# Optimization experiments

Hardware: AMD Instinct MI355X
Metric: run time of the kernel (lower is better)

## Reference

```python
import jax, jax.numpy as jnp
from jax import lax
import numpy as np

RANK = 128
INPUT_DIM = 128
OUT_DIM = 32
N = 128
L = 512
INIT_STD = 1.0 / np.sqrt(RANK * INPUT_DIM)  # variance-preserving recurrence


def setup_inputs() -> dict:
    key = jax.random.key(0)
    k_x, k_A, k_a, k_O = jax.random.split(key, 4)
    x = jax.random.normal(k_x, (N, L, INPUT_DIM), dtype=jnp.float32)
    A = INIT_STD * jax.random.normal(k_A, (RANK, INPUT_DIM, RANK), dtype=jnp.float32)
    alpha = INIT_STD * jax.random.normal(k_a, (RANK,), dtype=jnp.float32)
    Omega = INIT_STD * jax.random.normal(k_O, (RANK, OUT_DIM), dtype=jnp.float32)
    return {"x": x, "alpha": alpha, "A": A, "Omega": Omega}


def reference(x, alpha, A, Omega):
    # x: [N, L, D]; alpha: [R]; A: [R, D, R]; Omega: [R, M]
    # h_0 = einsum('i,ijk,nj->nk', alpha, A, x[:,0])
    h0 = jnp.einsum('i,ijk,nj->nk', alpha, A, x[:, 0, :])

    def step(h, xt):
        # h: [N, R], xt: [N, D] -> new h: [N, R]
        h = jnp.einsum('ni,ijk,nj->nk', h, A, xt)
        return h, None

    xs = jnp.swapaxes(x, 0, 1)[1:]  # [L-1, N, D]
    h, _ = lax.scan(step, h0, xs)
    out = jnp.einsum('ni,im->nm', h, Omega)  # [N, M]
    return jnp.squeeze(out)
```

## Files before the change

### kernel.cpp

```cpp
#include <hip/hip_runtime.h>

typedef _Float16 f16;
typedef _Float16 half8 __attribute__((ext_vector_type(8)));
typedef _Float16 half4v __attribute__((ext_vector_type(4)));
typedef float f32x4 __attribute__((ext_vector_type(4)));


#define GLOAD_LDS16(g, l) __builtin_amdgcn_global_load_lds( \
    (const __attribute__((address_space(1))) void*)(g),     \
    (__attribute__((address_space(3))) void*)(l), 16, 0, 0)

__global__ void k_cvt_pre(const float* __restrict__ x, f16* __restrict__ Xh,
                          const float* __restrict__ A, f16* __restrict__ Af2) {
    int b = blockIdx.x;
    if (b < 256) {
        int tid = (b << 8) + threadIdx.x;
        int n = tid >> 9;
        int rem = tid & 511;
        int off = (n << 16) + (rem << 2);
        float4 v = *(const float4*)(x + off);
        half4v o; o[0] = (f16)v.x; o[1] = (f16)v.y; o[2] = (f16)v.z; o[3] = (f16)v.w;
        *(half4v*)(Xh + off) = o;
    } else {
        int o = ((b - 256) << 8) + threadIdx.x;
        int i = o >> 14, k = (o >> 7) & 127, j = o & 127;
        Af2[o] = (f16)A[(i << 14) + (j << 7) + k];
    }
}

__device__ __forceinline__
void gemm_body(f16* lA, f16* lX, const f16* __restrict__ Af2, const f16* __restrict__ Xh,
               f16* __restrict__ B, int t0, int logTc, int qtile, int i, int tid) {
    const int Tcm1 = (1 << logTc) - 1;
    const int rowidx = tid >> 4;
    const int cc = tid & 15;
    const int scc = cc ^ rowidx;
    const int wv = tid >> 6;

    {
        const f16* srcA = Af2 + ((size_t)i << 14);
#pragma unroll
        for (int r = 0; r < 128; r += 16) {
            GLOAD_LDS16(srcA + ((r + rowidx) << 7) + (scc << 3),
                        lA + ((r + (wv << 2)) << 7));
        }
#pragma unroll
        for (int r = 0; r < 128; r += 16) {
            int qr = (qtile << 7) + r + rowidx;
            int n = qr >> logTc;
            int trel = qr & Tcm1;
            GLOAD_LDS16(Xh + (((size_t)(n << 9) + t0 + trel) << 7) + (scc << 3),
                        lX + ((r + (wv << 2)) << 7));
        }
    }
    __syncthreads();

    const int lane = tid & 63;
    const int l15 = lane & 15;
    const int l4 = lane >> 4;
    f32x4 acc[8][2] = {};

#pragma unroll
    for (int ks = 0; ks < 4; ++ks) {
        const int c = (ks << 2) + l4;
        half8 afr[8], bfr[2];
#pragma unroll
        for (int mt = 0; mt < 8; ++mt) {
            int rowA = (mt << 4) + l15;
            afr[mt] = *(const half8*)(&lA[(rowA << 7) + ((c ^ l15) << 3)]);
        }
#pragma unroll
        for (int qt = 0; qt < 2; ++qt) {
            int rowX = (wv << 5) + (qt << 4) + l15;
            bfr[qt] = *(const half8*)(&lX[(rowX << 7) + ((c ^ l15) << 3)]);
        }
#pragma unroll
        for (int mt = 0; mt < 8; ++mt)
#pragma unroll
            for (int qt = 0; qt < 2; ++qt)
                acc[mt][qt] = __builtin_amdgcn_mfma_f32_16x16x32_f16(
                    afr[mt], bfr[qt], acc[mt][qt], 0, 0, 0);
    }

    __syncthreads();
    f16* stage = lA;
#pragma unroll
    for (int mt = 0; mt < 8; ++mt)
#pragma unroll
        for (int qt = 0; qt < 2; ++qt) {
            int q = (wv << 5) + (qt << 4) + l15;
            int chunk = (mt << 1) + (l4 >> 1);
            int hf = l4 & 1;
            half4v o;
            o[0] = (f16)acc[mt][qt][0];
            o[1] = (f16)acc[mt][qt][1];
            o[2] = (f16)acc[mt][qt][2];
            o[3] = (f16)acc[mt][qt][3];
            *(half4v*)(&stage[(q << 7) + (((chunk ^ l15) << 3) + (hf << 2))]) = o;
        }
    __syncthreads();
    {
        const int lr = lane >> 4;
        const int lc = lane & 15;
#pragma unroll
        for (int it = 0; it < 8; ++it) {
            int q = (wv << 5) + (it << 2) + lr;
            uint4 v = *(const uint4*)(&stage[(q << 7) + ((lc ^ (q & 15)) << 3)]);
            size_t qg = (size_t)((qtile << 7) + q);
            *(uint4*)(B + (qg << 14) + (i << 7) + (lc << 3)) = v;
        }
    }
}

__device__ __forceinline__
void chain_body(float* hl, float (*part)[132], const f16* __restrict__ B,
                float* __restrict__ hstate, const float* __restrict__ alpha,
                const float* __restrict__ Om, float* __restrict__ out,
                int Tc, int first, int last, int n, int tid) {
    const int kg = tid & 15;
    const int iq = tid >> 4;

    if (tid < 128) hl[tid] = first ? alpha[tid] : hstate[(n << 7) + tid];
    __syncthreads();

    const f16* bbase = B + (((size_t)n * Tc) << 14) + (iq << 10) + (kg << 3);
    half8 buf[4][8];
#pragma unroll
    for (int s = 0; s < 4; ++s)
#pragma unroll
        for (int ii = 0; ii < 8; ++ii)
            buf[s][ii] = *(const half8*)(bbase + ((size_t)s << 14) + (ii << 7));

    for (int t = 0; t < Tc; t += 4) {
#pragma unroll
        for (int s = 0; s < 4; ++s) {
            float4 h0 = *(const float4*)&hl[iq << 3];
            float4 h1 = *(const float4*)&hl[(iq << 3) + 4];
            float acc[8] = {0, 0, 0, 0, 0, 0, 0, 0};
#pragma unroll
            for (int ii = 0; ii < 4; ++ii) {
                float hv = (&h0.x)[ii];
#pragma unroll
                for (int j = 0; j < 8; ++j)
                    acc[j] += hv * (float)buf[s][ii][j];
            }
#pragma unroll
            for (int ii = 0; ii < 4; ++ii) {
                float hv = (&h1.x)[ii];
#pragma unroll
                for (int j = 0; j < 8; ++j)
                    acc[j] += hv * (float)buf[s][ii + 4][j];
            }
            int tn = t + s + 4;
            if (tn < Tc) {
#pragma unroll
                for (int ii = 0; ii < 8; ++ii)
                    buf[s][ii] = *(const half8*)(bbase + ((size_t)tn << 14) + (ii << 7));
            }
            *(float4*)(&part[iq][kg << 3])       = make_float4(acc[0], acc[1], acc[2], acc[3]);
            *(float4*)(&part[iq][(kg << 3) + 4]) = make_float4(acc[4], acc[5], acc[6], acc[7]);
            __syncthreads();
            if (tid < 128) {
                float s0 = part[0][tid] + part[1][tid];
                float s1 = part[2][tid] + part[3][tid];
                float s2 = part[4][tid] + part[5][tid];
                float s3 = part[6][tid] + part[7][tid];
                s0 += part[8][tid] + part[9][tid];
                s1 += part[10][tid] + part[11][tid];
                s2 += part[12][tid] + part[13][tid];
                s3 += part[14][tid] + part[15][tid];
                hl[tid] = (s0 + s1) + (s2 + s3);
            }
            __syncthreads();
        }
    }

    if (!last) {
        if (tid < 128) hstate[(n << 7) + tid] = hl[tid];
    } else if (tid < 32) {
        float s = 0.f;
        for (int i2 = 0; i2 < 128; ++i2) s += hl[i2] * Om[(i2 << 5) + tid];
        out[(n << 5) + tid] = s;
    }
}

__device__ __forceinline__ int chain_n(int bx, int logTc) {
    if (logTc == 4) return (bx & 64) | ((bx & 7) << 3) | ((bx >> 3) & 7);
    return bx;
}

__global__ __launch_bounds__(256, 2)
void k_gemm0(const f16* __restrict__ Af2, const f16* __restrict__ Xh,
             f16* __restrict__ B, const float* __restrict__ x, int logTc) {
    __shared__ __align__(16) char smem[65536];
    const int bx = blockIdx.x;
    const int Tc = 1 << logTc;
    const int ngemm = Tc << 7;
    if (bx < ngemm) {
        gemm_body((f16*)smem, (f16*)(smem + 32768), Af2, Xh, B, 0, logTc,
                  bx & (Tc - 1), bx >> logTc, threadIdx.x);
    } else {
        int f = ((bx - ngemm) << 8) + threadIdx.x;
        int t = (f & 16383) >> 5;
        if (t < 16) return;
        float4 v = *(const float4*)(x + ((size_t)f << 2));
        half4v o; o[0] = (f16)v.x; o[1] = (f16)v.y; o[2] = (f16)v.z; o[3] = (f16)v.w;
        *(half4v*)(Xh + ((size_t)f << 2)) = o;
    }
}

__global__ __launch_bounds__(256, 2)
void k_chain(const f16* __restrict__ B, float* __restrict__ hstate,
             const float* __restrict__ alpha, const float* __restrict__ Om,
             float* __restrict__ out, int Tc, int logTc, int first, int last) {
    __shared__ __align__(16) char smem[16384];
    chain_body((float*)smem, (float(*)[132])(smem + 512), B, hstate, alpha, Om, out,
               Tc, first, last, chain_n(blockIdx.x, logTc), threadIdx.x);
}

__global__ __launch_bounds__(256, 2)
void k_fused(const f16* __restrict__ Af2, const f16* __restrict__ Xh,
             f16* __restrict__ Bw, const f16* __restrict__ Br,
             float* __restrict__ hstate, const float* __restrict__ alpha,
             const float* __restrict__ Om, float* __restrict__ out,
             int t0g, int logTc, int Tc, int first, int last) {
    __shared__ __align__(16) char smem[65536];
    const int bx = blockIdx.x;
    if (bx < 128) {
        chain_body((float*)smem, (float(*)[132])(smem + 512), Br, hstate, alpha, Om, out,
                   Tc, first, last, chain_n(bx, logTc), threadIdx.x);
    } else {
        int g = bx - 128;
        int qtile = g & (Tc - 1);
        int i = g >> logTc;
        gemm_body((f16*)smem, (f16*)(smem + 32768), Af2, Xh, Bw, t0g, logTc,
                  qtile, i, threadIdx.x);
    }
}

extern "C" void kernel_launch(void* const* d_in, const int* in_sizes, int n_in,
                              void* d_out, int out_size, void* d_ws, size_t ws_size,
                              hipStream_t stream) {
    const float* x     = (const float*)d_in[0];
    const float* alpha = (const float*)d_in[1];
    const float* A     = (const float*)d_in[2];
    const float* Om    = (const float*)d_in[3];
    float* out = (float*)d_out;

    char* ws = (char*)d_ws;
    f16*   Af2    = (f16*)ws;
    f16*   Xh     = (f16*)(ws + ((size_t)4 << 20));
    float* hstate = (float*)(ws + ((size_t)20 << 20));

    int Tc = 16;
    while (Tc > 4 && ((size_t)21 << 20) + (((size_t)Tc << 22) * 2) > ws_size) Tc >>= 1;
    int logTc = 31 - __builtin_clz(Tc);
    int nch = 512 / Tc;
    f16* Bc[2];
    Bc[0] = (f16*)(ws + ((size_t)21 << 20));
    Bc[1] = (f16*)(ws + ((size_t)21 << 20) + ((size_t)Tc << 22));

    k_cvt_pre<<<256 + 8192, 256, 0, stream>>>(x, Xh, A, Af2);
    k_gemm0<<<(Tc << 7) + 8192, 256, 0, stream>>>(Af2, Xh, Bc[0], x, logTc);

    for (int c = 0; c < nch; ++c) {
        const f16* br = Bc[c & 1];
        if (c + 1 < nch) {
            k_fused<<<128 + Tc * 128, 256, 0, stream>>>(
                Af2, Xh, Bc[(c + 1) & 1], br, hstate, alpha, Om, out,
                (c + 1) * Tc, logTc, Tc, c == 0, c == nch - 1);
        } else {
            k_chain<<<128, 256, 0, stream>>>(br, hstate, alpha, Om, out,
                                             Tc, logTc, c == 0, c == nch - 1);
        }
    }
    (void)in_sizes; (void)n_in; (void)out_size;
}
```

Baseline: 964.7 us.

## Load GEMM operands directly from global into MFMA registers, halve LDS, raise occupancy

The GEMM body no longer stages the A slice and X tile through LDS with global_load_lds. Each lane now reads its half8 MFMA fragments straight from global memory, so the kernel needs half the shared memory, which is used only for output staging. Launch bounds go from 2 to 4 blocks per CU. This removes the LDS fill and barrier, but each A fragment is now read from global/L2 by every wave instead of once per block, and the higher occupancy target may limit registers and cause spills.

New measurement: 2.355 ms. 144% more time.

```diff
diff --git a/kernel.cpp b/kernel.cpp
--- a/kernel.cpp
+++ b/kernel.cpp
@@ -5,10 +5,6 @@
 typedef _Float16 half4v __attribute__((ext_vector_type(4)));
 typedef float f32x4 __attribute__((ext_vector_type(4)));
 
-
-#define GLOAD_LDS16(g, l) __builtin_amdgcn_global_load_lds( \
-    (const __attribute__((address_space(1))) void*)(g),     \
-    (__attribute__((address_space(3))) void*)(l), 16, 0, 0)
 
 __global__ void k_cvt_pre(const float* __restrict__ x, f16* __restrict__ Xh,
                           const float* __restrict__ A, f16* __restrict__ Af2) {
@@ -29,51 +25,34 @@
 }
 
 __device__ __forceinline__
-void gemm_body(f16* lA, f16* lX, const f16* __restrict__ Af2, const f16* __restrict__ Xh,
+void gemm_body(f16* stage, const f16* __restrict__ Af2, const f16* __restrict__ Xh,
                f16* __restrict__ B, int t0, int logTc, int qtile, int i, int tid) {
     const int Tcm1 = (1 << logTc) - 1;
-    const int rowidx = tid >> 4;
-    const int cc = tid & 15;
-    const int scc = cc ^ rowidx;
     const int wv = tid >> 6;
-
-    {
-        const f16* srcA = Af2 + ((size_t)i << 14);
-#pragma unroll
-        for (int r = 0; r < 128; r += 16) {
-            GLOAD_LDS16(srcA + ((r + rowidx) << 7) + (scc << 3),
-                        lA + ((r + (wv << 2)) << 7));
-        }
-#pragma unroll
-        for (int r = 0; r < 128; r += 16) {
-            int qr = (qtile << 7) + r + rowidx;
-            int n = qr >> logTc;
-            int trel = qr & Tcm1;
-            GLOAD_LDS16(Xh + (((size_t)(n << 9) + t0 + trel) << 7) + (scc << 3),
-                        lX + ((r + (wv << 2)) << 7));
-        }
-    }
-    __syncthreads();
-
     const int lane = tid & 63;
     const int l15 = lane & 15;
     const int l4 = lane >> 4;
+
+    const f16* arow = Af2 + ((size_t)i << 14) + (l15 << 7);
+    const f16* xrow[2];
+#pragma unroll
+    for (int qt = 0; qt < 2; ++qt) {
+        int qr = (qtile << 7) + (wv << 5) + (qt << 4) + l15;
+        int n = qr >> logTc;
+        xrow[qt] = Xh + (((size_t)(n << 9) + t0 + (qr & Tcm1)) << 7);
+    }
+
     f32x4 acc[8][2] = {};
-
 #pragma unroll
     for (int ks = 0; ks < 4; ++ks) {
-        const int c = (ks << 2) + l4;
+        const int c8 = (((ks << 2) + l4) << 3);
         half8 afr[8], bfr[2];
 #pragma unroll
-        for (int mt = 0; mt < 8; ++mt) {
-            int rowA = (mt << 4) + l15;
-            afr[mt] = *(const half8*)(&lA[(rowA << 7) + ((c ^ l15) << 3)]);
-        }
-#pragma unroll
-        for (int qt = 0; qt < 2; ++qt) {
-            int rowX = (wv << 5) + (qt << 4) + l15;
-            bfr[qt] = *(const half8*)(&lX[(rowX << 7) + ((c ^ l15) << 3)]);
-        }
+        for (int mt = 0; mt < 8; ++mt)
+            afr[mt] = *(const half8*)(arow + (mt << 11) + c8);
+#pragma unroll
+        for (int qt = 0; qt < 2; ++qt)
+            bfr[qt] = *(const half8*)(xrow[qt] + c8);
 #pragma unroll
         for (int mt = 0; mt < 8; ++mt)
 #pragma unroll
@@ -83,7 +62,6 @@
     }
 
     __syncthreads();
-    f16* stage = lA;
 #pragma unroll
     for (int mt = 0; mt < 8; ++mt)
 #pragma unroll
@@ -189,15 +167,15 @@
     return bx;
 }
 
-__global__ __launch_bounds__(256, 2)
+__global__ __launch_bounds__(256, 4)
 void k_gemm0(const f16* __restrict__ Af2, const f16* __restrict__ Xh,
              f16* __restrict__ B, const float* __restrict__ x, int logTc) {
-    __shared__ __align__(16) char smem[65536];
+    __shared__ __align__(16) char smem[32768];
     const int bx = blockIdx.x;
     const int Tc = 1 << logTc;
     const int ngemm = Tc << 7;
     if (bx < ngemm) {
-        gemm_body((f16*)smem, (f16*)(smem + 32768), Af2, Xh, B, 0, logTc,
+        gemm_body((f16*)smem, Af2, Xh, B, 0, logTc,
                   bx & (Tc - 1), bx >> logTc, threadIdx.x);
     } else {
         int f = ((bx - ngemm) << 8) + threadIdx.x;
@@ -209,7 +187,7 @@
     }
 }
 
-__global__ __launch_bounds__(256, 2)
+__global__ __launch_bounds__(256, 4)
 void k_chain(const f16* __restrict__ B, float* __restrict__ hstate,
              const float* __restrict__ alpha, const float* __restrict__ Om,
              float* __restrict__ out, int Tc, int logTc, int first, int last) {
@@ -218,13 +196,13 @@
                Tc, first, last, chain_n(blockIdx.x, logTc), threadIdx.x);
 }
 
-__global__ __launch_bounds__(256, 2)
+__global__ __launch_bounds__(256, 4)
 void k_fused(const f16* __restrict__ Af2, const f16* __restrict__ Xh,
              f16* __restrict__ Bw, const f16* __restrict__ Br,
              float* __restrict__ hstate, const float* __restrict__ alpha,
              const float* __restrict__ Om, float* __restrict__ out,
              int t0g, int logTc, int Tc, int first, int last) {
-    __shared__ __align__(16) char smem[65536];
+    __shared__ __align__(16) char smem[32768];
     const int bx = blockIdx.x;
     if (bx < 128) {
         chain_body((float*)smem, (float(*)[132])(smem + 512), Br, hstate, alpha, Om, out,
@@ -233,8 +211,7 @@
         int g = bx - 128;
         int qtile = g & (Tc - 1);
         int i = g >> logTc;
-        gemm_body((f16*)smem, (f16*)(smem + 32768), Af2, Xh, Bw, t0g, logTc,
-                  qtile, i, threadIdx.x);
+        gemm_body((f16*)smem, Af2, Xh, Bw, t0g, logTc, qtile, i, threadIdx.x);
     }
 }
 
```
